# Optimization experiments

Measured on AMD Instinct MI355X. Metric: run time of the kernel, lower is better.

Reference implementation:

```python
import jax, jax.numpy as jnp
import numpy as np

N = 100000
E = 1600000
IN_DIM, HID_DIM, OUT_DIM = 128, 64, 32
HEADS = 8
NEG_SLOPE = 0.2
NEG_INF = -1e9


def _glorot(key, shape):
    stdv = np.sqrt(6.0 / (shape[-2] + shape[-1]))
    return jax.random.uniform(key, shape, jnp.float32, -stdv, stdv)


def gat_conv(x, src, dst, self_mask, W, att, bias, heads, out_ch, concat):
    """One GATConv layer (eval mode: dropout off). src/dst already include self-loops;
    self_mask marks original edges that were self-loops (removed via -inf score)."""
    n = x.shape[0]
    h = (x @ W).reshape(n, heads, out_ch)              # [N,H,C]
    x_i = h[dst]                                        # [Etot,H,C] gather target
    x_j = h[src]                                        # [Etot,H,C] gather source
    a = jnp.einsum('ehc,hc->eh', x_i, att[0, :, :out_ch]) \
        + jnp.einsum('ehc,hc->eh', x_j, att[0, :, out_ch:])
    alpha = jax.nn.leaky_relu(a, NEG_SLOPE)             # [Etot,H]
    alpha = jnp.where(self_mask[:, None], NEG_INF, alpha)
    amax = jax.lax.stop_gradient(
        jax.ops.segment_max(alpha, dst, num_segments=n))
    ex = jnp.exp(alpha - amax[dst])
    denom = jax.ops.segment_sum(ex, dst, num_segments=n)
    w = ex / denom[dst]                                 # segment softmax over incoming edges
    out = jax.ops.segment_sum(x_j * w[:, :, None], dst, num_segments=n)  # [N,H,C]
    out = out.reshape(n, heads * out_ch) if concat else out.mean(axis=1)
    return out + bias


def setup_inputs() -> dict:
    key = jax.random.key(0)
    ks = jax.random.split(key, 12)
    x = jax.random.normal(ks[0], (N, IN_DIM), jnp.float32)
    edge_index = jax.random.randint(ks[1], (2, E), 0, N, jnp.int64)
    c1 = HID_DIM // HEADS  # 8
    params = {
        'W1': _glorot(ks[2], (IN_DIM, HEADS * c1)),
        'att1': _glorot(ks[3], (1, HEADS, 2 * c1)),
        'b1': jnp.zeros((HID_DIM,), jnp.float32),
        'W2': _glorot(ks[4], (HID_DIM, HEADS * c1)),
        'att2': _glorot(ks[5], (1, HEADS, 2 * c1)),
        'b2': jnp.zeros((HID_DIM,), jnp.float32),
        'W3': _glorot(ks[6], (HID_DIM, 1 * OUT_DIM)),
        'att3': _glorot(ks[7], (1, 1, 2 * OUT_DIM)),
        'b3': jnp.zeros((OUT_DIM,), jnp.float32),
    }
    return dict(x=x, edge_index=edge_index, **params)


def reference(x, edge_index, W1, att1, b1, W2, att2, b2, W3, att3, b3):
    n = x.shape[0]
    src, dst = edge_index[0], edge_index[1]
    loop = jnp.arange(n, dtype=src.dtype)
    src_f = jnp.concatenate([src, loop])
    dst_f = jnp.concatenate([dst, loop])
    # remove_self_loops + add_self_loops: mask original self-loops, append fresh ones
    self_mask = jnp.concatenate([src == dst, jnp.zeros((n,), bool)])
    c1 = HID_DIM // HEADS
    h = jax.nn.elu(gat_conv(x, src_f, dst_f, self_mask, W1, att1, b1, HEADS, c1, True))
    h = jax.nn.elu(gat_conv(h, src_f, dst_f, self_mask, W2, att2, b2, HEADS, c1, True))
    out = gat_conv(h, src_f, dst_f, self_mask, W3, att3, b3, 1, OUT_DIM, False)
    return out
```

## Files before the change

### kernel.cpp

```cpp
#include <hip/hip_runtime.h>
#include <hip/hip_bf16.h>

#define NN 100000
#define EE 1600000

constexpr int SCAN_BLK = 1024;
constexpr int NB_SCAN  = (NN + SCAN_BLK - 1) / SCAN_BLK;

constexpr int NR2 = 8;
constexpr int RSZ = NN / NR2;
constexpr int CH  = 32;
constexpr int CSZ = EE / CH;


__global__ __launch_bounds__(256) void histL_k(const int* __restrict__ ei,
                                               int* __restrict__ CntG) {
    __shared__ int cnt[RSZ];
    int r = blockIdx.x % NR2, c = blockIdx.x / NR2;
    int lo = r * RSZ;
    for (int t = threadIdx.x; t < RSZ; t += 256) cnt[t] = 0;
    __syncthreads();
    const int* __restrict__ dstp = ei + EE;
    int base = c * CSZ;
    int tid = threadIdx.x;
    for (int ii = 0; ii < CSZ; ii += 1024) {
        int d[4], s[4];
        #pragma unroll
        for (int k = 0; k < 4; ++k) {
            int off = ii + tid + k * 256;
            bool v = off < CSZ;
            d[k] = v ? dstp[base + off] : -1;
            s[k] = v ? ei[base + off]   : -1;
        }
        #pragma unroll
        for (int k = 0; k < 4; ++k) {
            int dl = d[k] - lo;
            if (dl >= 0 && dl < RSZ && s[k] != d[k]) atomicAdd(&cnt[dl], 1);
        }
    }
    __syncthreads();
    for (int t = threadIdx.x; t < RSZ; t += 256)
        CntG[(size_t)c * NN + lo + t] = cnt[t];
}

__global__ void combineL_k(int* __restrict__ CntG, int* __restrict__ deg) {
    int d = blockIdx.x * 256 + threadIdx.x;
    if (d < NN) {
        int run = 0;
        #pragma unroll 8
        for (int c = 0; c < CH; ++c) {
            int v = CntG[(size_t)c * NN + d];
            CntG[(size_t)c * NN + d] = run;
            run += v;
        }
        deg[d] = run;
    }
}

__global__ void sum_blocks(const int* __restrict__ deg, int* __restrict__ partials) {
    __shared__ int sh[256];
    int t = threadIdx.x;
    int base = blockIdx.x * SCAN_BLK + t * 4;
    int s = 0;
    #pragma unroll
    for (int k = 0; k < 4; ++k) { int i = base + k; if (i < NN) s += deg[i]; }
    sh[t] = s; __syncthreads();
    for (int off = 128; off > 0; off >>= 1) {
        if (t < off) sh[t] += sh[t + off];
        __syncthreads();
    }
    if (t == 0) partials[blockIdx.x] = sh[0];
}

__global__ void scan_partials(int* __restrict__ partials) {
    __shared__ int sh[128];
    int t = threadIdx.x;
    int v = (t < NB_SCAN) ? partials[t] : 0;
    sh[t] = v;
    __syncthreads();
    for (int off = 1; off < 128; off <<= 1) {
        int tmp = (t >= off) ? sh[t - off] : 0;
        __syncthreads();
        sh[t] += tmp;
        __syncthreads();
    }
    if (t < NB_SCAN) partials[t] = sh[t] - v;
}

__global__ void scan_final(const int* __restrict__ deg, const int* __restrict__ partials,
                           int* __restrict__ rowptr) {
    __shared__ int sh[256];
    int t = threadIdx.x;
    int base = blockIdx.x * SCAN_BLK + t * 4;
    int v[4]; int s = 0;
    #pragma unroll
    for (int k = 0; k < 4; ++k) { int i = base + k; v[k] = (i < NN) ? deg[i] : 0; s += v[k]; }
    sh[t] = s; __syncthreads();
    for (int off = 1; off < 256; off <<= 1) {
        int tmp = (t >= off) ? sh[t - off] : 0;
        __syncthreads();
        sh[t] += tmp;
        __syncthreads();
    }
    int pref = partials[blockIdx.x] + sh[t] - s;
    #pragma unroll
    for (int k = 0; k < 4; ++k) {
        int i = base + k;
        if (i < NN) {
            rowptr[i] = pref; pref += v[k];
            if (i == NN - 1) rowptr[NN] = pref;
        }
    }
}

__global__ __launch_bounds__(256) void scatterL_k(const int* __restrict__ ei,
                                                  const int* __restrict__ CntG,
                                                  const int* __restrict__ rowptr,
                                                  int* __restrict__ col) {
    __shared__ int cur[RSZ];
    int r = blockIdx.x % NR2, c = blockIdx.x / NR2;
    int lo = r * RSZ;
    for (int t = threadIdx.x; t < RSZ; t += 256)
        cur[t] = rowptr[lo + t] + CntG[(size_t)c * NN + lo + t];
    __syncthreads();
    const int* __restrict__ dstp = ei + EE;
    int base = c * CSZ;
    int tid = threadIdx.x;
    for (int ii = 0; ii < CSZ; ii += 1024) {
        int d[4], s[4];
        #pragma unroll
        for (int k = 0; k < 4; ++k) {
            int off = ii + tid + k * 256;
            bool v = off < CSZ;
            d[k] = v ? dstp[base + off] : -1;
            s[k] = v ? ei[base + off]   : -1;
        }
        #pragma unroll
        for (int k = 0; k < 4; ++k) {
            int dl = d[k] - lo;
            if (dl >= 0 && dl < RSZ && s[k] != d[k]) {
                int p = atomicAdd(&cur[dl], 1);
                col[p] = s[k];
            }
        }
    }
}


template<int K, int M, int H, int NPB>
__global__ __launch_bounds__(256) void gemm_tile(const float* __restrict__ xin,
                          const float* __restrict__ W,
                          const float* __restrict__ att,
                          uint2* __restrict__ Hbf,
                          float* __restrict__ ssrcA,
                          float* __restrict__ sdst) {
    constexpr int C   = M / H;
    constexpr int MG  = M / 4;
    constexpr int NG  = NPB / 4;
    static_assert(MG * NG == 256, "tile mismatch");
    constexpr int K4  = K / 4;
    constexpr int KC4 = (K4 > 16) ? 16 : K4;
    constexpr int NCH = K4 / KC4;

    __shared__ float4 Wq[K * MG];
    __shared__ float4 Xq[NPB * KC4];

    int tid = threadIdx.x;
    const float4* W4 = (const float4*)W;
    for (int i = tid; i < K * MG; i += 256) Wq[i] = W4[i];

    int node0 = blockIdx.x * NPB;
    const float4* x4 = (const float4*)xin;

    int mg = tid % MG, ng = tid / MG;
    int nb = ng * 4;
    float acc[4][4];
    #pragma unroll
    for (int i = 0; i < 4; ++i)
        #pragma unroll
        for (int j = 0; j < 4; ++j) acc[i][j] = 0.f;

    for (int ch = 0; ch < NCH; ++ch) {
        __syncthreads();
        for (int i = tid; i < NPB * KC4; i += 256) {
            int n = i / KC4, k4l = i % KC4;
            int node = node0 + n;
            float4 v = make_float4(0.f, 0.f, 0.f, 0.f);
            if (node < NN) v = x4[(size_t)node * K4 + ch * KC4 + k4l];
            Xq[i] = v;
        }
        __syncthreads();
        #pragma unroll 4
        for (int k4 = 0; k4 < KC4; ++k4) {
            float4 xv[4], wv[4];
            #pragma unroll
            for (int i = 0; i < 4; ++i) xv[i] = Xq[(nb + i) * KC4 + k4];
            int kbase = (ch * KC4 + k4) * 4;
            #pragma unroll
            for (int kk = 0; kk < 4; ++kk) wv[kk] = Wq[(kbase + kk) * MG + mg];
            #pragma unroll
            for (int i = 0; i < 4; ++i) {
                const float* xf = (const float*)&xv[i];
                #pragma unroll
                for (int kk = 0; kk < 4; ++kk) {
                    const float* wf = (const float*)&wv[kk];
                    float xs = xf[kk];
                    acc[i][0] = fmaf(xs, wf[0], acc[i][0]);
                    acc[i][1] = fmaf(xs, wf[1], acc[i][1]);
                    acc[i][2] = fmaf(xs, wf[2], acc[i][2]);
                    acc[i][3] = fmaf(xs, wf[3], acc[i][3]);
                }
            }
        }
    }

    constexpr int TPH = C / 4;
    int head = mg / TPH;
    int c0   = (mg % TPH) * 4;
    float ad[4], as_[4];
    #pragma unroll
    for (int j = 0; j < 4; ++j) {
        ad[j]  = att[head * 2 * C + c0 + j];
        as_[j] = att[head * 2 * C + C + c0 + j];
    }
    #pragma unroll
    for (int i = 0; i < 4; ++i) {
        int node = node0 + nb + i;
        if (node < NN) {
            unsigned short us[4];
            #pragma unroll
            for (int j = 0; j < 4; ++j) {
                __hip_bfloat16 b = __float2bfloat16(acc[i][j]);
                us[j] = *(unsigned short*)&b;
            }
            uint2 pk;
            pk.x = (unsigned)us[0] | ((unsigned)us[1] << 16);
            pk.y = (unsigned)us[2] | ((unsigned)us[3] << 16);
            Hbf[(size_t)node * MG + mg] = pk;
        }
        float pd = acc[i][0]*ad[0]  + acc[i][1]*ad[1]  + acc[i][2]*ad[2]  + acc[i][3]*ad[3];
        float ps = acc[i][0]*as_[0] + acc[i][1]*as_[1] + acc[i][2]*as_[2] + acc[i][3]*as_[3];
        #pragma unroll
        for (int off = 1; off < TPH; off <<= 1) {
            pd += __shfl_xor(pd, off, 64);
            ps += __shfl_xor(ps, off, 64);
        }
        if ((mg % TPH) == 0 && node < NN) {
            sdst[node * H + head]  = pd;
            ssrcA[node * H + head] = ps;
        }
    }
}


template<int CT, int H, int U, bool ELU_OUT>
__global__ __launch_bounds__(256) void agg_k(const int* __restrict__ rowptr, const int* __restrict__ col,
                      const float* __restrict__ sdst, const float* __restrict__ ssrcA,
                      const uint2* __restrict__ Hbf,
                      const float* __restrict__ bias, float* __restrict__ output) {
    constexpr int C    = CT / H;
    constexpr int CP   = CT / 4;
    constexpr int G    = 64 / CP;
    constexpr int NL   = U / G;
    constexpr int EPEL = (U * H >= 64) ? (U * H) / 64 : 1;
    static_assert(EPEL == 1 || EPEL == 2, "mapping");

    int lane = threadIdx.x & 63;
    int node = blockIdx.x * (blockDim.x >> 6) + (threadIdx.x >> 6);
    if (node >= NN) return;

    int cp = lane % CP;
    int pp = lane / CP;
    int hh = (4 * cp) / C;
    int eh = lane % H;
    int gb = lane / H;
    bool elane = (lane < U * H);

    float sd = elane ? sdst[node * H + eh] : 0.f;

    int start = rowptr[node], end = rowptr[node + 1];

    float dsum = 0.f;
    float e_self = 0.f;
    if (lane < H) {
        float ss = ssrcA[node * H + lane];
        float a = sd + ss; a = (a >= 0.f) ? a : 0.2f * a;
        e_self = __expf(a);
        dsum = e_self;
    }
    uint2 hs = Hbf[(size_t)node * CP + cp];
    float exs = __shfl(e_self, hh, 64);
    float4 acc = make_float4(0.f, 0.f, 0.f, 0.f);
    if (pp == 0) {
        acc.x = exs * __uint_as_float(hs.x << 16);
        acc.y = exs * __uint_as_float(hs.x & 0xffff0000u);
        acc.z = exs * __uint_as_float(hs.y << 16);
        acc.w = exs * __uint_as_float(hs.y & 0xffff0000u);
    }

    int cv = node;
    if (start < end) {
        int idx = start + lane;
        if (lane < U && idx < end) cv = col[idx];
    }

    for (int j = start; j < end; j += U) {
        float s1 = 0.f, s2 = 0.f;
        int b1 = 0, b2 = 0;
        if (EPEL == 2) {
            b1 = __shfl(cv, gb, 64);
            b2 = __shfl(cv, gb + U / 2, 64);
            s1 = ssrcA[b1 * H + eh];
            s2 = ssrcA[b2 * H + eh];
        } else {
            b1 = __shfl(cv, gb, 64);
            if (elane) s1 = ssrcA[b1 * H + eh];
        }

        uint2 hv[NL];
        #pragma unroll
        for (int t = 0; t < NL; ++t) {
            int se = __shfl(cv, t * G + pp, 64);
            hv[t] = Hbf[(size_t)se * CP + cp];
        }

        int jn = j + U;
        int cvN = node;
        if (jn < end) {
            int idx = jn + lane;
            if (lane < U && idx < end) cvN = col[idx];
        }

        float e1 = 0.f, e2 = 0.f;
        if (EPEL == 2) {
            float a1 = sd + s1; a1 = (a1 >= 0.f) ? a1 : 0.2f * a1;
            float a2 = sd + s2; a2 = (a2 >= 0.f) ? a2 : 0.2f * a2;
            if (j + gb < end)         e1 = __expf(a1);
            if (j + gb + U / 2 < end) e2 = __expf(a2);
            dsum += e1 + e2;
        } else {
            float a1 = sd + s1; a1 = (a1 >= 0.f) ? a1 : 0.2f * a1;
            if (elane && j + gb < end) { e1 = __expf(a1); dsum += e1; }
        }

        #pragma unroll
        for (int t = 0; t < NL; ++t) {
            int eidx = t * G + pp;
            float ex;
            if (EPEL == 2)
                ex = __shfl((t * G + G - 1 < U / 2) ? e1 : e2, (eidx & (U / 2 - 1)) * H + hh, 64);
            else
                ex = __shfl(e1, eidx * H + hh, 64);
            float f0 = __uint_as_float(hv[t].x << 16);
            float f1 = __uint_as_float(hv[t].x & 0xffff0000u);
            float f2 = __uint_as_float(hv[t].y << 16);
            float f3 = __uint_as_float(hv[t].y & 0xffff0000u);
            acc.x = fmaf(ex, f0, acc.x);
            acc.y = fmaf(ex, f1, acc.y);
            acc.z = fmaf(ex, f2, acc.z);
            acc.w = fmaf(ex, f3, acc.w);
        }
        cv = cvN;
    }

    #pragma unroll
    for (int off = H; off < 64; off <<= 1) dsum += __shfl_xor(dsum, off, 64);
    float den = __shfl(dsum, hh, 64);
    #pragma unroll
    for (int off = CP; off < 64; off <<= 1) {
        acc.x += __shfl_xor(acc.x, off, 64);
        acc.y += __shfl_xor(acc.y, off, 64);
        acc.z += __shfl_xor(acc.z, off, 64);
        acc.w += __shfl_xor(acc.w, off, 64);
    }
    if (lane < CP) {
        float inv = 1.f / den;
        float4 bv = ((const float4*)bias)[cp];
        float4 v;
        v.x = acc.x * inv + bv.x;
        v.y = acc.y * inv + bv.y;
        v.z = acc.z * inv + bv.z;
        v.w = acc.w * inv + bv.w;
        if (ELU_OUT) {
            v.x = (v.x > 0.f) ? v.x : expm1f(v.x);
            v.y = (v.y > 0.f) ? v.y : expm1f(v.y);
            v.z = (v.z > 0.f) ? v.z : expm1f(v.z);
            v.w = (v.w > 0.f) ? v.w : expm1f(v.w);
        }
        ((float4*)output)[(size_t)node * CP + cp] = v;
    }
}


extern "C" void kernel_launch(void* const* d_in, const int* in_sizes, int n_in,
                              void* d_out, int out_size, void* d_ws, size_t ws_size,
                              hipStream_t stream) {
    const float* x    = (const float*)d_in[0];
    const int*   ei   = (const int*)d_in[1];
    const float* W1   = (const float*)d_in[2];
    const float* att1 = (const float*)d_in[3];
    const float* b1   = (const float*)d_in[4];
    const float* W2   = (const float*)d_in[5];
    const float* att2 = (const float*)d_in[6];
    const float* b2   = (const float*)d_in[7];
    const float* W3   = (const float*)d_in[8];
    const float* att3 = (const float*)d_in[9];
    const float* b3   = (const float*)d_in[10];
    float* out = (float*)d_out;

    char* p = (char*)d_ws;
    auto alloc = [&](size_t bytes) -> void* {
        void* r = (void*)p;
        p += (bytes + 255) & ~(size_t)255;
        return r;
    };
    int*   rowptr   = (int*)alloc((NN + 1) * sizeof(int));
    int*   deg      = (int*)alloc(NN * sizeof(int));
    int*   CntG     = (int*)alloc((size_t)CH * NN * sizeof(int));
    int*   partials = (int*)alloc(NB_SCAN * sizeof(int));
    int*   col      = (int*)alloc(EE * sizeof(int));
    float* sdst     = (float*)alloc((size_t)NN * 8 * sizeof(float));
    float* ssrcA    = (float*)alloc((size_t)NN * 8 * sizeof(float));
    uint2* Hbf      = (uint2*)alloc((size_t)NN * 16 * sizeof(uint2));
    float* Fb       = (float*)alloc((size_t)NN * 64 * sizeof(float));

    histL_k<<<CH * NR2, 256, 0, stream>>>(ei, CntG);
    combineL_k<<<(NN + 255) / 256, 256, 0, stream>>>(CntG, deg);
    sum_blocks<<<NB_SCAN, 256, 0, stream>>>(deg, partials);
    scan_partials<<<1, 128, 0, stream>>>(partials);
    scan_final<<<NB_SCAN, 256, 0, stream>>>(deg, partials, rowptr);
    scatterL_k<<<CH * NR2, 256, 0, stream>>>(ei, CntG, rowptr, col);

    gemm_tile<128, 64, 8, 64><<<(NN + 63) / 64, 256, 0, stream>>>(x, W1, att1, Hbf, ssrcA, sdst);
    agg_k<64, 8, 16, true><<<(NN + 3) / 4, 256, 0, stream>>>(rowptr, col, sdst, ssrcA, Hbf, b1, Fb);

    gemm_tile<64, 64, 8, 64><<<(NN + 63) / 64, 256, 0, stream>>>(Fb, W2, att2, Hbf, ssrcA, sdst);
    agg_k<64, 8, 16, true><<<(NN + 3) / 4, 256, 0, stream>>>(rowptr, col, sdst, ssrcA, Hbf, b2, Fb);

    gemm_tile<64, 32, 1, 128><<<(NN + 127) / 128, 256, 0, stream>>>(Fb, W3, att3, Hbf, ssrcA, sdst);
    agg_k<32, 1, 32, false><<<(NN + 3) / 4, 256, 0, stream>>>(rowptr, col, sdst, ssrcA, Hbf, b3, out);
}
```

Before: 422.6 us.

## Replace LDS-partitioned CSR build with global-atomic degree count and scatter

Swaps the two-pass shared-memory histogram (8 node ranges by 32 edge chunks, each block rescanning its chunk) for direct global atomics on degree and cursor arrays. One thread handles each edge once, which removes the 8x redundant edge reads, the 32xN count buffer and the combine pass. In exchange it relies on contended global atomics and makes the column order within each row nondeterministic, which can change the floating-point summation order in aggregation.

```diff
diff --git a/kernel.cpp b/kernel.cpp
--- a/kernel.cpp
+++ b/kernel.cpp
@@ -7,53 +7,23 @@
 constexpr int SCAN_BLK = 1024;
 constexpr int NB_SCAN  = (NN + SCAN_BLK - 1) / SCAN_BLK;
 
-constexpr int NR2 = 8;
-constexpr int RSZ = NN / NR2;
-constexpr int CH  = 32;
-constexpr int CSZ = EE / CH;
-
-
-__global__ __launch_bounds__(256) void histL_k(const int* __restrict__ ei,
-                                               int* __restrict__ CntG) {
-    __shared__ int cnt[RSZ];
-    int r = blockIdx.x % NR2, c = blockIdx.x / NR2;
-    int lo = r * RSZ;
-    for (int t = threadIdx.x; t < RSZ; t += 256) cnt[t] = 0;
-    __syncthreads();
+
+__global__ void zero_deg(int* __restrict__ deg) {
+    int i = blockIdx.x * 256 + threadIdx.x;
+    if (i < NN) deg[i] = 0;
+}
+
+__global__ __launch_bounds__(256) void deg_atomic_k(const int* __restrict__ ei,
+                                                    int* __restrict__ deg) {
     const int* __restrict__ dstp = ei + EE;
-    int base = c * CSZ;
-    int tid = threadIdx.x;
-    for (int ii = 0; ii < CSZ; ii += 1024) {
-        int d[4], s[4];
-        #pragma unroll
-        for (int k = 0; k < 4; ++k) {
-            int off = ii + tid + k * 256;
-            bool v = off < CSZ;
-            d[k] = v ? dstp[base + off] : -1;
-            s[k] = v ? ei[base + off]   : -1;
-        }
-        #pragma unroll
-        for (int k = 0; k < 4; ++k) {
-            int dl = d[k] - lo;
-            if (dl >= 0 && dl < RSZ && s[k] != d[k]) atomicAdd(&cnt[dl], 1);
-        }
-    }
-    __syncthreads();
-    for (int t = threadIdx.x; t < RSZ; t += 256)
-        CntG[(size_t)c * NN + lo + t] = cnt[t];
-}
-
-__global__ void combineL_k(int* __restrict__ CntG, int* __restrict__ deg) {
-    int d = blockIdx.x * 256 + threadIdx.x;
-    if (d < NN) {
-        int run = 0;
-        #pragma unroll 8
-        for (int c = 0; c < CH; ++c) {
-            int v = CntG[(size_t)c * NN + d];
-            CntG[(size_t)c * NN + d] = run;
-            run += v;
-        }
-        deg[d] = run;
+    int base = blockIdx.x * 1024 + threadIdx.x;
+    #pragma unroll
+    for (int k = 0; k < 4; ++k) {
+        int off = base + k * 256;
+        if (off < EE) {
+            int s = ei[off], d = dstp[off];
+            if (s != d) atomicAdd(&deg[d], 1);
+        }
     }
 }
 
@@ -88,7 +58,7 @@
 }
 
 __global__ void scan_final(const int* __restrict__ deg, const int* __restrict__ partials,
-                           int* __restrict__ rowptr) {
+                           int* __restrict__ rowptr, int* __restrict__ cur) {
     __shared__ int sh[256];
     int t = threadIdx.x;
     int base = blockIdx.x * SCAN_BLK + t * 4;
@@ -107,40 +77,25 @@
     for (int k = 0; k < 4; ++k) {
         int i = base + k;
         if (i < NN) {
-            rowptr[i] = pref; pref += v[k];
+            rowptr[i] = pref; cur[i] = pref; pref += v[k];
             if (i == NN - 1) rowptr[NN] = pref;
         }
     }
 }
 
-__global__ __launch_bounds__(256) void scatterL_k(const int* __restrict__ ei,
-                                                  const int* __restrict__ CntG,
-                                                  const int* __restrict__ rowptr,
-                                                  int* __restrict__ col) {
-    __shared__ int cur[RSZ];
-    int r = blockIdx.x % NR2, c = blockIdx.x / NR2;
-    int lo = r * RSZ;
-    for (int t = threadIdx.x; t < RSZ; t += 256)
-        cur[t] = rowptr[lo + t] + CntG[(size_t)c * NN + lo + t];
-    __syncthreads();
+__global__ __launch_bounds__(256) void scatter_atomic_k(const int* __restrict__ ei,
+                                                        int* __restrict__ cur,
+                                                        int* __restrict__ col) {
     const int* __restrict__ dstp = ei + EE;
-    int base = c * CSZ;
-    int tid = threadIdx.x;
-    for (int ii = 0; ii < CSZ; ii += 1024) {
-        int d[4], s[4];
-        #pragma unroll
-        for (int k = 0; k < 4; ++k) {
-            int off = ii + tid + k * 256;
-            bool v = off < CSZ;
-            d[k] = v ? dstp[base + off] : -1;
-            s[k] = v ? ei[base + off]   : -1;
-        }
-        #pragma unroll
-        for (int k = 0; k < 4; ++k) {
-            int dl = d[k] - lo;
-            if (dl >= 0 && dl < RSZ && s[k] != d[k]) {
-                int p = atomicAdd(&cur[dl], 1);
-                col[p] = s[k];
+    int base = blockIdx.x * 1024 + threadIdx.x;
+    #pragma unroll
+    for (int k = 0; k < 4; ++k) {
+        int off = base + k * 256;
+        if (off < EE) {
+            int s = ei[off], d = dstp[off];
+            if (s != d) {
+                int p = atomicAdd(&cur[d], 1);
+                col[p] = s;
             }
         }
     }
@@ -416,7 +371,7 @@
     };
     int*   rowptr   = (int*)alloc((NN + 1) * sizeof(int));
     int*   deg      = (int*)alloc(NN * sizeof(int));
-    int*   CntG     = (int*)alloc((size_t)CH * NN * sizeof(int));
+    int*   cur      = (int*)alloc(NN * sizeof(int));
     int*   partials = (int*)alloc(NB_SCAN * sizeof(int));
     int*   col      = (int*)alloc(EE * sizeof(int));
     float* sdst     = (float*)alloc((size_t)NN * 8 * sizeof(float));
@@ -424,12 +379,12 @@
     uint2* Hbf      = (uint2*)alloc((size_t)NN * 16 * sizeof(uint2));
     float* Fb       = (float*)alloc((size_t)NN * 64 * sizeof(float));
 
-    histL_k<<<CH * NR2, 256, 0, stream>>>(ei, CntG);
-    combineL_k<<<(NN + 255) / 256, 256, 0, stream>>>(CntG, deg);
+    zero_deg<<<(NN + 255) / 256, 256, 0, stream>>>(deg);
+    deg_atomic_k<<<(EE + 1023) / 1024, 256, 0, stream>>>(ei, deg);
     sum_blocks<<<NB_SCAN, 256, 0, stream>>>(deg, partials);
     scan_partials<<<1, 128, 0, stream>>>(partials);
-    scan_final<<<NB_SCAN, 256, 0, stream>>>(deg, partials, rowptr);
-    scatterL_k<<<CH * NR2, 256, 0, stream>>>(ei, CntG, rowptr, col);
+    scan_final<<<NB_SCAN, 256, 0, stream>>>(deg, partials, rowptr, cur);
+    scatter_atomic_k<<<(EE + 1023) / 1024, 256, 0, stream>>>(ei, cur, col);
 
     gemm_tile<128, 64, 8, 64><<<(NN + 63) / 64, 256, 0, stream>>>(x, W1, att1, Hbf, ssrcA, sdst);
     agg_k<64, 8, 16, true><<<(NN + 3) / 4, 256, 0, stream>>>(rowptr, col, sdst, ssrcA, Hbf, b1, Fb);
```

Result: slower. 545.9 us (+29.2%).

## Fuse CSR build scan kernels and vectorize edge loads with int4

Applied to the files above, without the earlier changes.

Merges the per-chunk combine pass with the block-sum reduction into one kernel, and folds the single-block partials scan into every scan_final block, which removes two kernel launches from the CSR construction. The histogram and scatter kernels now read src/dst with int4 vector loads, four consecutive edges per thread, instead of four strided scalar loads. The combine kernel now runs far fewer blocks (NB_SCAN instead of NN/256), each handling four node groups, so it has less parallelism. Each scan_final block also redundantly rescans the partials array.

```diff
diff --git a/kernel.cpp b/kernel.cpp
--- a/kernel.cpp
+++ b/kernel.cpp
@@ -24,18 +24,15 @@
     int base = c * CSZ;
     int tid = threadIdx.x;
     for (int ii = 0; ii < CSZ; ii += 1024) {
-        int d[4], s[4];
-        #pragma unroll
-        for (int k = 0; k < 4; ++k) {
-            int off = ii + tid + k * 256;
-            bool v = off < CSZ;
-            d[k] = v ? dstp[base + off] : -1;
-            s[k] = v ? ei[base + off]   : -1;
-        }
-        #pragma unroll
-        for (int k = 0; k < 4; ++k) {
-            int dl = d[k] - lo;
-            if (dl >= 0 && dl < RSZ && s[k] != d[k]) atomicAdd(&cnt[dl], 1);
+        int off = ii + tid * 4;
+        if (off < CSZ) {
+            int4 s4 = *(const int4*)&ei[base + off];
+            int4 d4 = *(const int4*)&dstp[base + off];
+            int dl;
+            dl = d4.x - lo; if (dl >= 0 && dl < RSZ && s4.x != d4.x) atomicAdd(&cnt[dl], 1);
+            dl = d4.y - lo; if (dl >= 0 && dl < RSZ && s4.y != d4.y) atomicAdd(&cnt[dl], 1);
+            dl = d4.z - lo; if (dl >= 0 && dl < RSZ && s4.z != d4.z) atomicAdd(&cnt[dl], 1);
+            dl = d4.w - lo; if (dl >= 0 && dl < RSZ && s4.w != d4.w) atomicAdd(&cnt[dl], 1);
         }
     }
     __syncthreads();
@@ -43,54 +40,51 @@
         CntG[(size_t)c * NN + lo + t] = cnt[t];
 }
 
-__global__ void combineL_k(int* __restrict__ CntG, int* __restrict__ deg) {
-    int d = blockIdx.x * 256 + threadIdx.x;
-    if (d < NN) {
-        int run = 0;
-        #pragma unroll 8
-        for (int c = 0; c < CH; ++c) {
-            int v = CntG[(size_t)c * NN + d];
-            CntG[(size_t)c * NN + d] = run;
-            run += v;
-        }
-        deg[d] = run;
-    }
-}
-
-__global__ void sum_blocks(const int* __restrict__ deg, int* __restrict__ partials) {
+__global__ __launch_bounds__(256) void combine_sum_k(int* __restrict__ CntG,
+                                                     int* __restrict__ deg,
+                                                     int* __restrict__ partials) {
     __shared__ int sh[256];
     int t = threadIdx.x;
-    int base = blockIdx.x * SCAN_BLK + t * 4;
-    int s = 0;
-    #pragma unroll
-    for (int k = 0; k < 4; ++k) { int i = base + k; if (i < NN) s += deg[i]; }
-    sh[t] = s; __syncthreads();
+    int s_tot = 0;
+    #pragma unroll
+    for (int k = 0; k < 4; ++k) {
+        int d = blockIdx.x * SCAN_BLK + k * 256 + t;
+        int run = 0;
+        if (d < NN) {
+            #pragma unroll 8
+            for (int c = 0; c < CH; ++c) {
+                int v = CntG[(size_t)c * NN + d];
+                CntG[(size_t)c * NN + d] = run;
+                run += v;
+            }
+            deg[d] = run;
+        }
+        s_tot += run;
+    }
+    sh[t] = s_tot; __syncthreads();
     for (int off = 128; off > 0; off >>= 1) {
         if (t < off) sh[t] += sh[t + off];
         __syncthreads();
     }
     if (t == 0) partials[blockIdx.x] = sh[0];
-}
-
-__global__ void scan_partials(int* __restrict__ partials) {
-    __shared__ int sh[128];
-    int t = threadIdx.x;
-    int v = (t < NB_SCAN) ? partials[t] : 0;
-    sh[t] = v;
-    __syncthreads();
-    for (int off = 1; off < 128; off <<= 1) {
-        int tmp = (t >= off) ? sh[t - off] : 0;
-        __syncthreads();
-        sh[t] += tmp;
-        __syncthreads();
-    }
-    if (t < NB_SCAN) partials[t] = sh[t] - v;
 }
 
 __global__ void scan_final(const int* __restrict__ deg, const int* __restrict__ partials,
                            int* __restrict__ rowptr) {
     __shared__ int sh[256];
+    __shared__ int sp[128];
     int t = threadIdx.x;
+    if (t < 128) sp[t] = (t < NB_SCAN) ? partials[t] : 0;
+    __syncthreads();
+    for (int off = 1; off < 128; off <<= 1) {
+        int tmp = 0;
+        if (t < 128 && t >= off) tmp = sp[t - off];
+        __syncthreads();
+        if (t < 128) sp[t] += tmp;
+        __syncthreads();
+    }
+    int pref0 = sp[blockIdx.x] - partials[blockIdx.x];
+
     int base = blockIdx.x * SCAN_BLK + t * 4;
     int v[4]; int s = 0;
     #pragma unroll
@@ -102,7 +96,7 @@
         sh[t] += tmp;
         __syncthreads();
     }
-    int pref = partials[blockIdx.x] + sh[t] - s;
+    int pref = pref0 + sh[t] - s;
     #pragma unroll
     for (int k = 0; k < 4; ++k) {
         int i = base + k;
@@ -127,21 +121,15 @@
     int base = c * CSZ;
     int tid = threadIdx.x;
     for (int ii = 0; ii < CSZ; ii += 1024) {
-        int d[4], s[4];
-        #pragma unroll
-        for (int k = 0; k < 4; ++k) {
-            int off = ii + tid + k * 256;
-            bool v = off < CSZ;
-            d[k] = v ? dstp[base + off] : -1;
-            s[k] = v ? ei[base + off]   : -1;
-        }
-        #pragma unroll
-        for (int k = 0; k < 4; ++k) {
-            int dl = d[k] - lo;
-            if (dl >= 0 && dl < RSZ && s[k] != d[k]) {
-                int p = atomicAdd(&cur[dl], 1);
-                col[p] = s[k];
-            }
+        int off = ii + tid * 4;
+        if (off < CSZ) {
+            int4 s4 = *(const int4*)&ei[base + off];
+            int4 d4 = *(const int4*)&dstp[base + off];
+            int dl;
+            dl = d4.x - lo; if (dl >= 0 && dl < RSZ && s4.x != d4.x) { int p = atomicAdd(&cur[dl], 1); col[p] = s4.x; }
+            dl = d4.y - lo; if (dl >= 0 && dl < RSZ && s4.y != d4.y) { int p = atomicAdd(&cur[dl], 1); col[p] = s4.y; }
+            dl = d4.z - lo; if (dl >= 0 && dl < RSZ && s4.z != d4.z) { int p = atomicAdd(&cur[dl], 1); col[p] = s4.z; }
+            dl = d4.w - lo; if (dl >= 0 && dl < RSZ && s4.w != d4.w) { int p = atomicAdd(&cur[dl], 1); col[p] = s4.w; }
         }
     }
 }
@@ -425,9 +413,7 @@
     float* Fb       = (float*)alloc((size_t)NN * 64 * sizeof(float));
 
     histL_k<<<CH * NR2, 256, 0, stream>>>(ei, CntG);
-    combineL_k<<<(NN + 255) / 256, 256, 0, stream>>>(CntG, deg);
-    sum_blocks<<<NB_SCAN, 256, 0, stream>>>(deg, partials);
-    scan_partials<<<1, 128, 0, stream>>>(partials);
+    combine_sum_k<<<NB_SCAN, 256, 0, stream>>>(CntG, deg, partials);
     scan_final<<<NB_SCAN, 256, 0, stream>>>(deg, partials, rowptr);
     scatterL_k<<<CH * NR2, 256, 0, stream>>>(ei, CntG, rowptr, col);
 
```

Result: faster. 410.6 us (-2.8%).
